# Kernel tuning notes

Measured on AMD Instinct MI355X. Metric: run time of the kernel, lower is better.

The kernel has to match this reference:

```python
import jax, jax.numpy as jnp
import numpy as np

C = 128

def setup_inputs() -> dict:
    key = jax.random.key(0)
    ks = jax.random.split(key, 8)
    x = jax.random.normal(ks[0], (8, C, 64, 64), dtype=jnp.float32)
    y = jax.random.normal(ks[1], (8, C, 32, 32), dtype=jnp.float32)
    s = 1.0 / np.sqrt(C)
    Wq = jax.random.normal(ks[2], (C, C), dtype=jnp.float32) * s
    bq = jnp.zeros((C,), dtype=jnp.float32)
    Wk = jax.random.normal(ks[3], (C, C), dtype=jnp.float32) * s
    bk = jnp.zeros((C,), dtype=jnp.float32)
    Wv = jax.random.normal(ks[4], (C, C), dtype=jnp.float32) * s
    bv = jnp.zeros((C,), dtype=jnp.float32)
    return {"x": x, "y": y, "Wq": Wq, "bq": bq, "Wk": Wk, "bk": bk, "Wv": Wv, "bv": bv}


def reference(x, y, Wq, bq, Wk, bk, Wv, bv):
    B, C_, H, W = x.shape
    # flatten spatial -> tokens: (B, N, C)
    x_flat = x.reshape(B, C_, H * W).transpose(0, 2, 1)
    y_flat = y.reshape(B, C_, -1).transpose(0, 2, 1)
    # torch Linear: out = in @ W.T + b
    Q = jnp.einsum('bnc,dc->bnd', x_flat, Wq) + bq
    K = jnp.einsum('bmc,dc->bmd', y_flat, Wk) + bk
    V = jnp.einsum('bmc,dc->bmd', y_flat, Wv) + bv
    scale = 1.0 / jnp.sqrt(jnp.asarray(C_, dtype=x.dtype))
    scores = jnp.einsum('bnd,bmd->bnm', Q, K) * scale  # (B, HW, H'W')
    attn = jax.nn.softmax(scores, axis=-1)
    z = jnp.einsum('bnm,bmd->bnd', attn, V)
    z = z.transpose(0, 2, 1).reshape(B, C_, H, W)
    return x + z
```

## Files before the change

### kernel.cpp

```cpp
#include <hip/hip_runtime.h>

#define BB 8
#define NN 4096
#define MMK 1024
#define SMAX 2.0f
#define SCL 0.0883883476483184f

typedef __bf16 v8bf __attribute__((ext_vector_type(8)));
typedef float v4f __attribute__((ext_vector_type(4)));
typedef float v16f __attribute__((ext_vector_type(16)));
#define MFMA16 __builtin_amdgcn_mfma_f32_16x16x32_bf16
#define MFMA32F8 __builtin_amdgcn_mfma_f32_32x32x16_fp8_fp8

static __device__ __forceinline__ unsigned pk4(float a, float b, float c, float d) {
    int u = __builtin_amdgcn_cvt_pk_fp8_f32(a, b, 0, false);
    u = __builtin_amdgcn_cvt_pk_fp8_f32(c, d, u, true);
    return (unsigned)u;
}
static __device__ __forceinline__ long long mk64(unsigned lo, unsigned hi) {
    return (long long)(((unsigned long long)hi << 32) | lo);
}
static __device__ __forceinline__ long long lo64(uint4 u) { return mk64(u.x, u.y); }
static __device__ __forceinline__ long long hi64(uint4 u) { return mk64(u.z, u.w); }

#define COMPUTE_S(DST, KB)                                                  \
    do {                                                                    \
        v16f a1, a2;                                                        \
        _Pragma("unroll")                                                   \
        for (int r_ = 0; r_ < 16; ++r_) { a1[r_] = 0.f; a2[r_] = 0.f; }     \
        a1 = MFMA32F8(lo64(KB[0]), lo64(qv[0]), a1, 0, 0, 0);               \
        a2 = MFMA32F8(lo64(KB[2]), lo64(qv[2]), a2, 0, 0, 0);               \
        a1 = MFMA32F8(hi64(KB[0]), hi64(qv[0]), a1, 0, 0, 0);               \
        a2 = MFMA32F8(hi64(KB[2]), hi64(qv[2]), a2, 0, 0, 0);               \
        a1 = MFMA32F8(lo64(KB[1]), lo64(qv[1]), a1, 0, 0, 0);               \
        a2 = MFMA32F8(lo64(KB[3]), lo64(qv[3]), a2, 0, 0, 0);               \
        a1 = MFMA32F8(hi64(KB[1]), hi64(qv[1]), a1, 0, 0, 0);               \
        a2 = MFMA32F8(hi64(KB[3]), hi64(qv[3]), a2, 0, 0, 0);               \
        _Pragma("unroll")                                                   \
        for (int r_ = 0; r_ < 16; ++r_) DST[r_] = a1[r_] + a2[r_];          \
    } while (0)

#define XTS 68
__global__ __launch_bounds__(256, 1) void proj(
    const float* __restrict__ x, const float* __restrict__ y,
    const float* __restrict__ Wq, const float* __restrict__ bq,
    const float* __restrict__ Wk, const float* __restrict__ bk,
    const float* __restrict__ Wv, const float* __restrict__ bv,
    unsigned char* __restrict__ Qfr, unsigned char* __restrict__ Kfr,
    unsigned char* __restrict__ Vfr)
{
    __shared__ __align__(16) __bf16 xt[128 * XTS];
    __shared__ float bsh[128];

    const int tid = threadIdx.x;
    const int wave = tid >> 6, lane = tid & 63, l15 = lane & 15, quad = lane >> 4;
    const int bid = blockIdx.x;

    int job, b, t0, stride;
    const float *in, *W, *bias;
    if (bid < 512)      { job = 0; b = bid >> 6;         t0 = (bid & 63) * 64;         in = x; stride = NN;  W = Wq; bias = bq; }
    else if (bid < 640) { job = 1; b = (bid - 512) >> 4; t0 = ((bid - 512) & 15) * 64; in = y; stride = MMK; W = Wk; bias = bk; }
    else                { job = 2; b = (bid - 640) >> 4; t0 = ((bid - 640) & 15) * 64; in = y; stride = MMK; W = Wv; bias = bv; }

    #pragma unroll
    for (int i = 0; i < 8; ++i) {
        const int s = i * 256 + tid;
        const int c = s >> 4, c4 = s & 15;
        float4 v = *(const float4*)(in + (size_t)(b * 128 + c) * stride + t0 + c4 * 4);
        union { __bf16 h[4]; uint2 u; } o;
        o.h[0] = (__bf16)v.x; o.h[1] = (__bf16)v.y; o.h[2] = (__bf16)v.z; o.h[3] = (__bf16)v.w;
        *(uint2*)(xt + c * XTS + c4 * 4) = o.u;
    }
    if (tid < 128) bsh[tid] = bias[tid];
    __syncthreads();

    v8bf xf[4];
    {
        const int tok = wave * 16 + l15;
        #pragma unroll
        for (int cg = 0; cg < 4; ++cg) {
            union { __bf16 h[8]; v8bf v; } u;
            #pragma unroll
            for (int jj = 0; jj < 8; ++jj)
                u.h[jj] = xt[(cg * 32 + quad * 8 + jj) * XTS + tok];
            xf[cg] = u.v;
        }
    }

    for (int dg = 0; dg < 8; ++dg) {
        v8bf wf[4];
        #pragma unroll
        for (int cg = 0; cg < 4; ++cg) {
            const float* wp = W + (size_t)(dg * 16 + l15) * 128 + cg * 32 + quad * 8;
            float4 a = *(const float4*)wp;
            float4 c2 = *(const float4*)(wp + 4);
            union { __bf16 h[8]; v8bf v; } u;
            u.h[0] = (__bf16)a.x;  u.h[1] = (__bf16)a.y;  u.h[2] = (__bf16)a.z;  u.h[3] = (__bf16)a.w;
            u.h[4] = (__bf16)c2.x; u.h[5] = (__bf16)c2.y; u.h[6] = (__bf16)c2.z; u.h[7] = (__bf16)c2.w;
            wf[cg] = u.v;
        }
        v4f acc;
        #pragma unroll
        for (int r = 0; r < 4; ++r) acc[r] = bsh[dg * 16 + quad * 4 + r];
        #pragma unroll
        for (int cg = 0; cg < 4; ++cg)
            acc = MFMA16(wf[cg], xf[cg], acc, 0, 0, 0);

        const int tok = t0 + wave * 16 + l15;
        const int d0 = dg * 16 + quad * 4;
        const unsigned u32 = pk4(acc[0], acc[1], acc[2], acc[3]);

        if (job <= 1) {
            unsigned char* Out = (job == 0) ? Qfr : Kfr;
            const int tiles = (job == 0) ? 128 : 32;
            const size_t off = ((size_t)(b * tiles + (tok >> 5)) * 4 + (d0 >> 5)) * 1024
                             + ((d0 >> 3) & 1) * 512 + (tok & 31) * 16
                             + ((d0 >> 4) & 1) * 8 + (d0 & 7);
            *(unsigned*)(Out + off) = u32;
        } else {
            #pragma unroll
            for (int r = 0; r < 4; ++r) {
                const int ch = d0 + r, key = tok;
                const size_t off = ((size_t)(b * 32 + (key >> 5)) * 4 + (ch >> 5)) * 1024
                                 + ((key >> 3) & 1) * 512 + (ch & 31) * 16
                                 + ((key >> 4) & 1) * 8 + (key & 7);
                Vfr[off] = (unsigned char)(u32 >> (8 * r));
            }
        }
    }
}

__global__ __launch_bounds__(128, 2) void attn(
    const float* __restrict__ x, const unsigned char* __restrict__ Qfr,
    const unsigned char* __restrict__ Kfr, const unsigned char* __restrict__ Vfr,
    float* __restrict__ out)
{
    __shared__ float Oacc[128 * 32];
    __shared__ float Lacc[2][32];

    const int tid = threadIdx.x;
    const int wave = tid >> 6, lane = tid & 63, r31 = lane & 31, h = lane >> 5;
    const int b = blockIdx.x >> 7;
    const int qt = blockIdx.x & 127;

    const uint4* Qc = (const uint4*)Qfr + (size_t)(b * 128 + qt) * 4 * 64;
    const uint4* Kc = (const uint4*)Kfr + (size_t)(b * 32 + wave * 16) * 4 * 64;
    const uint4* Vc = (const uint4*)Vfr + (size_t)(b * 32 + wave * 16) * 4 * 64;

    uint4 qv[4];
    #pragma unroll
    for (int s2 = 0; s2 < 4; ++s2) qv[s2] = Qc[s2 * 64 + lane];

    v16f o[4];
    #pragma unroll
    for (int cg = 0; cg < 4; ++cg)
        #pragma unroll
        for (int r = 0; r < 16; ++r) o[cg][r] = 0.f;
    float l0 = 0.f, l1 = 0.f, l2 = 0.f, l3 = 0.f;

    uint4 kb[2][4], vb[2][4];
    #pragma unroll
    for (int s2 = 0; s2 < 4; ++s2) kb[0][s2] = Kc[s2 * 64 + lane];
    #pragma unroll
    for (int s2 = 0; s2 < 4; ++s2) vb[0][s2] = Vc[s2 * 64 + lane];
    #pragma unroll
    for (int s2 = 0; s2 < 4; ++s2) kb[1][s2] = Kc[(4 + s2) * 64 + lane];
    #pragma unroll
    for (int s2 = 0; s2 < 4; ++s2) vb[1][s2] = Vc[(4 + s2) * 64 + lane];

    v16f S;
    COMPUTE_S(S, kb[0]);

    #pragma unroll
    for (int j = 0; j < 16; ++j) {
        const int cur = j & 1, nxt = (j + 1) & 1;

        if (j < 14) {
            #pragma unroll
            for (int s2 = 0; s2 < 4; ++s2)
                kb[cur][s2] = Kc[((j + 2) * 4 + s2) * 64 + lane];
        }

        float p[16];
        #pragma unroll
        for (int r = 0; r < 16; ++r) p[r] = __expf(fmaf(S[r], SCL, -SMAX));
        #pragma unroll
        for (int r = 0; r < 4; ++r) {
            l0 += p[r]; l1 += p[4 + r]; l2 += p[8 + r]; l3 += p[12 + r];
        }

        const unsigned qa = pk4(p[0], p[1], p[2], p[3]);
        const unsigned qb = pk4(p[4], p[5], p[6], p[7]);
        const unsigned qc = pk4(p[8], p[9], p[10], p[11]);
        const unsigned qd = pk4(p[12], p[13], p[14], p[15]);
        unsigned e0 = h ? qa : qb; e0 = __shfl_xor(e0, 32);
        unsigned e1 = h ? qc : qd; e1 = __shfl_xor(e1, 32);
        const long long pf0 = mk64(h ? e0 : qa, h ? qb : e0);
        const long long pf1 = mk64(h ? e1 : qc, h ? qd : e1);

        v16f Sn = S;
        if (j < 15) COMPUTE_S(Sn, kb[nxt]);

        #pragma unroll
        for (int cg = 0; cg < 4; ++cg) {
            o[cg] = MFMA32F8(lo64(vb[cur][cg]), pf0, o[cg], 0, 0, 0);
            o[cg] = MFMA32F8(hi64(vb[cur][cg]), pf1, o[cg], 0, 0, 0);
        }

        if (j < 14) {
            #pragma unroll
            for (int s2 = 0; s2 < 4; ++s2)
                vb[cur][s2] = Vc[((j + 2) * 4 + s2) * 64 + lane];
        }

        S = Sn;
    }

    float l = (l0 + l1) + (l2 + l3);
    l += __shfl_xor(l, 32);
    if (h == 0) Lacc[wave][r31] = l;
    if (wave == 0) {
        #pragma unroll
        for (int cg = 0; cg < 4; ++cg)
            #pragma unroll
            for (int r = 0; r < 16; ++r) {
                const int ch = cg * 32 + (r & 3) + 8 * (r >> 2) + 4 * h;
                Oacc[ch * 32 + r31] = o[cg][r];
            }
    }
    __syncthreads();
    if (wave == 1) {
        #pragma unroll
        for (int cg = 0; cg < 4; ++cg)
            #pragma unroll
            for (int r = 0; r < 16; ++r) {
                const int ch = cg * 32 + (r & 3) + 8 * (r >> 2) + 4 * h;
                Oacc[ch * 32 + r31] += o[cg][r];
            }
    }
    __syncthreads();

    const float linv = 1.0f / (Lacc[0][r31] + Lacc[1][r31]);

    #pragma unroll
    for (int i = 0; i < 32; ++i) {
        const int ch = (wave * 2 + h) + i * 4;
        const float val = Oacc[ch * 32 + r31] * linv;
        const size_t gi = (size_t)(b * 128 + ch) * NN + qt * 32 + r31;
        out[gi] = x[gi] + val;
    }
}

extern "C" void kernel_launch(void* const* d_in, const int* in_sizes, int n_in,
                              void* d_out, int out_size, void* d_ws, size_t ws_size,
                              hipStream_t stream) {
    const float* x  = (const float*)d_in[0];
    const float* y  = (const float*)d_in[1];
    const float* Wq = (const float*)d_in[2];
    const float* bq = (const float*)d_in[3];
    const float* Wk = (const float*)d_in[4];
    const float* bk = (const float*)d_in[5];
    const float* Wv = (const float*)d_in[6];
    const float* bv = (const float*)d_in[7];
    float* out = (float*)d_out;

    unsigned char* Qfr = (unsigned char*)d_ws;
    unsigned char* Kfr = Qfr + (size_t)BB * NN * 128;
    unsigned char* Vfr = Kfr + (size_t)BB * MMK * 128;

    proj<<<768, 256, 0, stream>>>(x, y, Wq, bq, Wk, bk, Wv, bv, Qfr, Kfr, Vfr);
    attn<<<BB * (NN / 32), 128, 0, stream>>>(x, Qfr, Kfr, Vfr, out);
}
```

Baseline: 125.1 us.

## Stage projection weights in LDS, use exp2, permlane32 swap and MFMA priority

The projection kernel now converts the weight matrix to bf16 once into shared memory and reads the MFMA fragments from there, instead of reloading and converting fp32 weights from global memory for each output group. The softmax exponent is rewritten as a native exp2 with log2(e) folded into the scale and offset. The cross-half-wave exchange of P fragments uses permlane32_swap in place of select plus shuffle. s_setprio raises wave priority around the MFMA blocks. The extra 34 KB of LDS in the projection kernel may limit occupancy, and the correctness of the permlane swap ordering relies on the builtin's semantics.

```diff
diff --git a/kernel.cpp b/kernel.cpp
--- a/kernel.cpp
+++ b/kernel.cpp
@@ -3,8 +3,8 @@
 #define BB 8
 #define NN 4096
 #define MMK 1024
-#define SMAX 2.0f
-#define SCL 0.0883883476483184f
+#define SCLL2E 0.12751743f
+#define SM2 2.88539008f
 
 typedef __bf16 v8bf __attribute__((ext_vector_type(8)));
 typedef float v4f __attribute__((ext_vector_type(4)));
@@ -23,11 +23,22 @@
 static __device__ __forceinline__ long long lo64(uint4 u) { return mk64(u.x, u.y); }
 static __device__ __forceinline__ long long hi64(uint4 u) { return mk64(u.z, u.w); }
 
+static __device__ __forceinline__ float exp2_fast(float x) {
+#if __has_builtin(__builtin_amdgcn_exp2f)
+    return __builtin_amdgcn_exp2f(x);
+#else
+    float r;
+    asm("v_exp_f32 %0, %1" : "=v"(r) : "v"(x));
+    return r;
+#endif
+}
+
 #define COMPUTE_S(DST, KB)                                                  \
     do {                                                                    \
         v16f a1, a2;                                                        \
         _Pragma("unroll")                                                   \
         for (int r_ = 0; r_ < 16; ++r_) { a1[r_] = 0.f; a2[r_] = 0.f; }     \
+        __builtin_amdgcn_s_setprio(1);                                      \
         a1 = MFMA32F8(lo64(KB[0]), lo64(qv[0]), a1, 0, 0, 0);               \
         a2 = MFMA32F8(lo64(KB[2]), lo64(qv[2]), a2, 0, 0, 0);               \
         a1 = MFMA32F8(hi64(KB[0]), hi64(qv[0]), a1, 0, 0, 0);               \
@@ -36,11 +47,13 @@
         a2 = MFMA32F8(lo64(KB[3]), lo64(qv[3]), a2, 0, 0, 0);               \
         a1 = MFMA32F8(hi64(KB[1]), hi64(qv[1]), a1, 0, 0, 0);               \
         a2 = MFMA32F8(hi64(KB[3]), hi64(qv[3]), a2, 0, 0, 0);               \
+        __builtin_amdgcn_s_setprio(0);                                      \
         _Pragma("unroll")                                                   \
         for (int r_ = 0; r_ < 16; ++r_) DST[r_] = a1[r_] + a2[r_];          \
     } while (0)
 
 #define XTS 68
+#define WTS 136
 __global__ __launch_bounds__(256, 1) void proj(
     const float* __restrict__ x, const float* __restrict__ y,
     const float* __restrict__ Wq, const float* __restrict__ bq,
@@ -50,6 +63,7 @@
     unsigned char* __restrict__ Vfr)
 {
     __shared__ __align__(16) __bf16 xt[128 * XTS];
+    __shared__ __align__(16) __bf16 wt[128 * WTS];
     __shared__ float bsh[128];
 
     const int tid = threadIdx.x;
@@ -71,6 +85,15 @@
         o.h[0] = (__bf16)v.x; o.h[1] = (__bf16)v.y; o.h[2] = (__bf16)v.z; o.h[3] = (__bf16)v.w;
         *(uint2*)(xt + c * XTS + c4 * 4) = o.u;
     }
+    #pragma unroll
+    for (int i = 0; i < 16; ++i) {
+        const int f = i * 1024 + tid * 4;
+        const int d = f >> 7, c = f & 127;
+        float4 v = *(const float4*)(W + f);
+        union { __bf16 h[4]; uint2 u; } o;
+        o.h[0] = (__bf16)v.x; o.h[1] = (__bf16)v.y; o.h[2] = (__bf16)v.z; o.h[3] = (__bf16)v.w;
+        *(uint2*)(wt + d * WTS + c) = o.u;
+    }
     if (tid < 128) bsh[tid] = bias[tid];
     __syncthreads();
 
@@ -88,20 +111,15 @@
     }
 
     for (int dg = 0; dg < 8; ++dg) {
+        const __bf16* wrow = wt + (dg * 16 + l15) * WTS + quad * 8;
         v8bf wf[4];
         #pragma unroll
-        for (int cg = 0; cg < 4; ++cg) {
-            const float* wp = W + (size_t)(dg * 16 + l15) * 128 + cg * 32 + quad * 8;
-            float4 a = *(const float4*)wp;
-            float4 c2 = *(const float4*)(wp + 4);
-            union { __bf16 h[8]; v8bf v; } u;
-            u.h[0] = (__bf16)a.x;  u.h[1] = (__bf16)a.y;  u.h[2] = (__bf16)a.z;  u.h[3] = (__bf16)a.w;
-            u.h[4] = (__bf16)c2.x; u.h[5] = (__bf16)c2.y; u.h[6] = (__bf16)c2.z; u.h[7] = (__bf16)c2.w;
-            wf[cg] = u.v;
-        }
+        for (int cg = 0; cg < 4; ++cg)
+            wf[cg] = *(const v8bf*)(wrow + cg * 32);
+
+        float4 b4 = *(const float4*)(bsh + dg * 16 + quad * 4);
         v4f acc;
-        #pragma unroll
-        for (int r = 0; r < 4; ++r) acc[r] = bsh[dg * 16 + quad * 4 + r];
+        acc[0] = b4.x; acc[1] = b4.y; acc[2] = b4.z; acc[3] = b4.w;
         #pragma unroll
         for (int cg = 0; cg < 4; ++cg)
             acc = MFMA16(wf[cg], xf[cg], acc, 0, 0, 0);
@@ -183,7 +201,7 @@
 
         float p[16];
         #pragma unroll
-        for (int r = 0; r < 16; ++r) p[r] = __expf(fmaf(S[r], SCL, -SMAX));
+        for (int r = 0; r < 16; ++r) p[r] = exp2_fast(fmaf(S[r], SCLL2E, -SM2));
         #pragma unroll
         for (int r = 0; r < 4; ++r) {
             l0 += p[r]; l1 += p[4 + r]; l2 += p[8 + r]; l3 += p[12 + r];
@@ -193,19 +211,33 @@
         const unsigned qb = pk4(p[4], p[5], p[6], p[7]);
         const unsigned qc = pk4(p[8], p[9], p[10], p[11]);
         const unsigned qd = pk4(p[12], p[13], p[14], p[15]);
-        unsigned e0 = h ? qa : qb; e0 = __shfl_xor(e0, 32);
-        unsigned e1 = h ? qc : qd; e1 = __shfl_xor(e1, 32);
-        const long long pf0 = mk64(h ? e0 : qa, h ? qb : e0);
-        const long long pf1 = mk64(h ? e1 : qc, h ? qd : e1);
+        long long pf0, pf1;
+#if __has_builtin(__builtin_amdgcn_permlane32_swap)
+        {
+            auto r0 = __builtin_amdgcn_permlane32_swap((int)qa, (int)qb, false, false);
+            auto r1 = __builtin_amdgcn_permlane32_swap((int)qc, (int)qd, false, false);
+            pf0 = mk64((unsigned)r0[0], (unsigned)r0[1]);
+            pf1 = mk64((unsigned)r1[0], (unsigned)r1[1]);
+        }
+#else
+        {
+            unsigned e0 = h ? qa : qb; e0 = __shfl_xor(e0, 32);
+            unsigned e1 = h ? qc : qd; e1 = __shfl_xor(e1, 32);
+            pf0 = mk64(h ? e0 : qa, h ? qb : e0);
+            pf1 = mk64(h ? e1 : qc, h ? qd : e1);
+        }
+#endif
 
         v16f Sn = S;
         if (j < 15) COMPUTE_S(Sn, kb[nxt]);
 
+        __builtin_amdgcn_s_setprio(1);
         #pragma unroll
         for (int cg = 0; cg < 4; ++cg) {
             o[cg] = MFMA32F8(lo64(vb[cur][cg]), pf0, o[cg], 0, 0, 0);
             o[cg] = MFMA32F8(hi64(vb[cur][cg]), pf1, o[cg], 0, 0, 0);
         }
+        __builtin_amdgcn_s_setprio(0);
 
         if (j < 14) {
             #pragma unroll
```

After: 107.6 us. 14.0% less time.
